# Kernel tuning notes

Measured on AMD Instinct MI355X. Metric: run time of the kernel, lower is better.

The kernel has to match this reference:

```python
import jax, jax.numpy as jnp
import numpy as np

CUBE_LEN = 512
EQU_H = 1024
EQU_W = 2 * EQU_H
EQU_COUNT = 4
CHANNELS = 3


def _rodrigues(r):
    th = np.linalg.norm(r)
    if th < 1e-12:
        return np.eye(3)
    k = r / th
    K = np.array([[0.0, -k[2], k[1]], [k[2], 0.0, -k[0]], [-k[1], k[0], 0.0]])
    return np.eye(3) + np.sin(th) * K + (1.0 - np.cos(th)) * (K @ K)


def _build_lut(L, equ_h):
    # Identical math to Cube2Equirec.__init__/_intersection, fused into
    # per-pixel face id + per-pixel cube-face pixel coordinates (u, v).
    equ_w = equ_h * 2
    theta = (np.arange(equ_w) / (equ_w - 1) - 0.5) * 2 * np.pi
    phi = (np.arange(equ_h) / (equ_h - 1) - 0.5) * np.pi
    theta, phi = np.meshgrid(theta, phi)
    x = np.sin(theta) * np.cos(phi)
    y = np.sin(phi)
    z = np.cos(theta) * np.cos(phi)
    xyz = np.stack([x, y, z], axis=-1)  # [H, W, 3]
    planes = np.array([[0, 0, 1, -1], [1, 0, 0, -1], [0, 0, 1, 1],
                       [1, 0, 0, 1], [0, 1, 0, 1], [0, 1, 0, -1]], dtype=np.float64)
    r_lst = np.array([[0, 0, 0], [0, -0.5, 0], [0, 1, 0],
                      [0, 0.5, 0], [-0.5, 0, 0], [0.5, 0, 0]]) * np.pi
    f = L / 2.0
    K = np.array([[f, 0, (L - 1) / 2.0], [0, f, (L - 1) / 2.0], [0, 0, 1]])
    R_lst = np.stack([_rodrigues(r) for r in r_lst])  # [6, 3, 3]

    abc = planes[:, :3]
    with np.errstate(divide='ignore'):
        depth = -planes[:, 3][None, None, :] / (xyz @ abc.T)  # [H, W, 6]
    depth[depth < 0] = np.inf
    arg = np.argmin(depth, axis=-1)            # per-pixel face id
    dmin = np.min(depth, axis=-1)
    pts = dmin[..., None] * xyz                # intersection points
    Rs = R_lst[arg]                            # [H, W, 3, 3]
    proj = np.einsum('ij,hwjk,hwk->hwi', K, Rs, pts)  # K @ R @ pts
    uv = np.clip(proj[..., :2] / proj[..., 2:3], 0, L - 1)
    return uv.astype(np.float32), arg.astype(np.int32)


def setup_inputs() -> dict:
    key = jax.random.key(0)
    x = jax.random.normal(key, (6 * EQU_COUNT, CHANNELS, CUBE_LEN, CUBE_LEN),
                          dtype=jnp.float32)
    uv_np, face_np = _build_lut(CUBE_LEN, EQU_H)
    return {"x": x, "uv": jnp.asarray(uv_np), "face_idx": jnp.asarray(face_np)}


def _cube2equirec(x, uv, face_idx):
    # x: [6*E, C, L, L]; grid_sample(mode='bilinear', align_corners=True)
    # with grid = (uv/(L-1) - 0.5)*2 samples exactly at pixel coords uv.
    E6, C, L, _ = x.shape
    E = E6 // 6
    xr = x.reshape(E, 6, C, L, L)
    H, W = face_idx.shape
    f = face_idx.reshape(-1)                 # [N]
    u = uv[..., 0].reshape(-1)               # [N], in [0, L-1]
    v = uv[..., 1].reshape(-1)

    x0 = jnp.clip(jnp.floor(u).astype(jnp.int32), 0, L - 1)
    y0 = jnp.clip(jnp.floor(v).astype(jnp.int32), 0, L - 1)
    x1 = jnp.minimum(x0 + 1, L - 1)
    y1 = jnp.minimum(y0 + 1, L - 1)
    wx = (u - x0.astype(u.dtype))[:, None, None]  # [N,1,1]
    wy = (v - y0.astype(v.dtype))[:, None, None]

    def g(yy, xx):
        # advanced indices at axes 1,3,4 -> result [N, E, C]
        return xr[:, f, :, yy, xx]

    out = (g(y0, x0) * (1 - wx) * (1 - wy)
           + g(y0, x1) * wx * (1 - wy)
           + g(y1, x0) * (1 - wx) * wy
           + g(y1, x1) * wx * wy)              # [N, E, C]
    return jnp.transpose(out, (1, 2, 0)).reshape(E, C, H, W)


def reference(x, uv, face_idx):
    return _cube2equirec(x, uv, face_idx)
```

## Files before the change

kernel.cpp:

```cpp
#include <hip/hip_runtime.h>
#include <stdint.h>

#define EQU_H 1024
#define EQU_W 2048
#define HW (EQU_H * EQU_W)

typedef float f32x4 __attribute__((ext_vector_type(4)));
typedef float f32x2 __attribute__((ext_vector_type(2)));

#define IMG_OFF(i)  ((uint64_t)(((i) / 3) * 18874368u + ((i) % 3) * 1048576u))
#define IMG_FOFF(i) (((i) / 3) * 4718592 + ((i) % 3) * 262144)

__device__ __forceinline__ int wave_min(int v) {
#pragma unroll
    for (int o = 32; o; o >>= 1) v = min(v, __shfl_xor(v, o));
    return v;
}
__device__ __forceinline__ int wave_max(int v) {
#pragma unroll
    for (int o = 32; o; o >>= 1) v = max(v, __shfl_xor(v, o));
    return v;
}

__global__ __launch_bounds__(256, 1) void cube2equirec_kernel(
    const float* __restrict__ x,
    const float* __restrict__ uv,
    const int*   __restrict__ face,
    float*       __restrict__ out)
{
    __shared__ float slds[3][2048];
    __shared__ int   sred[24];

    const int tx = blockIdx.x & 63;
    const int ty = blockIdx.x >> 6;
    const int pr = threadIdx.x & 15;
    const int rw = threadIdx.x >> 4;
    const int w  = tx * 32 + pr * 2;
    const int h  = ty * 16 + rw;
    const int idx  = h * EQU_W + w;
    const int pidx = idx >> 1;

    const f32x4 uv4 = ((const f32x4*)uv)[pidx];
    const int2  fpr = ((const int2*)face)[pidx];
    const float uA = uv4.x, vA = uv4.y, uB = uv4.z, vB = uv4.w;
    const int   fA = fpr.x, fB = fpr.y;

    int x0A = (int)floorf(uA), y0A = (int)floorf(vA);
    int x0B = (int)floorf(uB), y0B = (int)floorf(vB);
    x0A = min(max(x0A, 0), 510); y0A = min(max(y0A, 0), 510);
    x0B = min(max(x0B, 0), 510); y0B = min(max(y0B, 0), 510);
    const float wxA = uA - (float)x0A, wyA = vA - (float)y0A;
    const float wxB = uB - (float)x0B, wyB = vB - (float)y0B;

    int fmn = min(fA, fB),   fmx = max(fA, fB);
    int xmn = min(x0A, x0B), xmx = max(x0A, x0B);
    int ymn = min(y0A, y0B), ymx = max(y0A, y0B);
    fmn = wave_min(fmn); fmx = wave_max(fmx);
    xmn = wave_min(xmn); xmx = wave_max(xmx);
    ymn = wave_min(ymn); ymx = wave_max(ymx);
    const int wid = threadIdx.x >> 6, lane = threadIdx.x & 63;
    if (lane == 0) {
        int* p = &sred[wid * 6];
        p[0] = fmn; p[1] = fmx; p[2] = xmn; p[3] = xmx; p[4] = ymn; p[5] = ymx;
    }
    __syncthreads();
#pragma unroll
    for (int ww = 0; ww < 4; ++ww) {
        const int* p = &sred[ww * 6];
        fmn = min(fmn, p[0]); fmx = max(fmx, p[1]);
        xmn = min(xmn, p[2]); xmx = max(xmx, p[3]);
        ymn = min(ymn, p[4]); ymx = max(ymx, p[5]);
    }

    const int  xs     = min(xmn & ~3, 448);
    const bool staged = (fmn == fmx) && ((xmx + 1 - xs) <= 63)
                                     && ((ymx - ymn) <= 29);
    const uint64_t xb = (uint64_t)x;

    if (staged) {
        const int R  = ymx + 2 - ymn;
        const int nu = R << 4;
        const float w00A = (1.f - wxA) * (1.f - wyA), w01A = wxA * (1.f - wyA);
        const float w10A = (1.f - wxA) * wyA,         w11A = wxA * wyA;
        const float w00B = (1.f - wxB) * (1.f - wyB), w01B = wxB * (1.f - wyB);
        const float w10B = (1.f - wxB) * wyB,         w11B = wxB * wyB;
        const int lA = ((y0A - ymn) << 6) + (x0A - xs);
        const int lB = ((y0B - ymn) << 6) + (x0B - xs);
        const int fbase = fmn * 786432;

#pragma unroll
        for (int k = 0; k < 4; ++k) {
#pragma unroll
            for (int r = 0; r < 3; ++r) {
                const float* src = x + IMG_FOFF(k * 3 + r) + fbase;
                int u = threadIdx.x;
                if (u < nu) {
                    const int row = u >> 4, c4 = (u & 15) << 2;
                    *((f32x4*)&slds[r][(row << 6) + c4]) =
                        *(const f32x4*)(src + (ymn + row) * 512 + xs + c4);
                }
                u += 256;
                if (u < nu) {
                    const int row = u >> 4, c4 = (u & 15) << 2;
                    *((f32x4*)&slds[r][(row << 6) + c4]) =
                        *(const f32x4*)(src + (ymn + row) * 512 + xs + c4);
                }
            }
            __syncthreads();
#pragma unroll
            for (int r = 0; r < 3; ++r) {
                const int i = k * 3 + r;
                const float* L = slds[r];
                const float a00 = L[lA], a01 = L[lA + 1];
                const float a10 = L[lA + 64], a11 = L[lA + 65];
                const float b00 = L[lB], b01 = L[lB + 1];
                const float b10 = L[lB + 64], b11 = L[lB + 65];
                f32x2 st;
                st.x = a00 * w00A + a01 * w01A + a10 * w10A + a11 * w11A;
                st.y = b00 * w00B + b01 * w01B + b10 * w10B + b11 * w11B;
                __builtin_nontemporal_store(st, (f32x2*)(out + (size_t)i * HW) + pidx);
            }
            __syncthreads();
        }
        return;
    }

    const int  xmw    = min(x0A, x0B);
    const bool compat = (fA == fB) && (y0A == y0B)
                     && ((max(x0A, x0B) - xmw) <= 2);
    const int xm  = min(compat ? xmw : x0A, 508);
    const int oAw = x0A - xm;
    const int oBw = min(max(x0B - xm, 0), 2);

    const uint32_t vbW = (uint32_t)(fA * 3145728 + y0A * 2048 + xm * 4);
    const uint32_t vbB = (uint32_t)(fB * 3145728 + y0B * 2048 + x0B * 4);

    const float aL = 1.f - wxA, aR = wxA;
    const float bL = 1.f - wxB, bR = wxB;
    f32x4 WA, WB;
    WA.x = (oAw == 0) ? aL : 0.f;
    WA.y = (oAw == 0) ? aR : ((oAw == 1) ? aL : 0.f);
    WA.z = (oAw == 2) ? aL : ((oAw == 1) ? aR : 0.f);
    WA.w = (oAw == 2) ? aR : 0.f;
    WB.x = (oBw == 0) ? bL : 0.f;
    WB.y = (oBw == 0) ? bR : ((oBw == 1) ? bL : 0.f);
    WB.z = (oBw == 2) ? bL : ((oBw == 1) ? bR : 0.f);
    WB.w = (oBw == 2) ? bR : 0.f;
    const f32x4 WA0 = WA * (1.f - wyA), WA1 = WA * wyA;
    const f32x4 WB0 = WB * (1.f - wyB), WB1 = WB * wyB;
    const float c00 = bL * (1.f - wyB), c01 = bR * (1.f - wyB);
    const float c10 = bL * wyB,         c11 = bR * wyB;

#define EMIT2(i, R0, R1, Q0, Q1)                                             \
    {                                                                        \
        const float ovA = R0.x * WA0.x + R0.y * WA0.y + R0.z * WA0.z         \
                        + R0.w * WA0.w + R1.x * WA1.x + R1.y * WA1.y         \
                        + R1.z * WA1.z + R1.w * WA1.w;                       \
        const float oBw2 = R0.x * WB0.x + R0.y * WB0.y + R0.z * WB0.z        \
                        + R0.w * WB0.w + R1.x * WB1.x + R1.y * WB1.y         \
                        + R1.z * WB1.z + R1.w * WB1.w;                       \
        const float oBf = Q0.x * c00 + Q0.y * c01 + Q1.x * c10 + Q1.y * c11; \
        f32x2 st;                                                            \
        st.x = ovA;                                                          \
        st.y = compat ? oBw2 : oBf;                                          \
        __builtin_nontemporal_store(st, (f32x2*)(out + (size_t)(i) * HW) + pidx); \
    }

#define ROUND(I0)                                                            \
    {                                                                        \
        f32x4 r0_0, r1_0, r0_1, r1_1, r0_2, r1_2,                            \
              r0_3, r1_3, r0_4, r1_4, r0_5, r1_5;                            \
        asm volatile(                                                        \
            "global_load_dwordx4 %[a0], %[vb], %[s0]\n\t"                    \
            "global_load_dwordx4 %[b0], %[vb], %[s0] offset:2048\n\t"        \
            "global_load_dwordx4 %[a1], %[vb], %[s1]\n\t"                    \
            "global_load_dwordx4 %[b1], %[vb], %[s1] offset:2048\n\t"        \
            "global_load_dwordx4 %[a2], %[vb], %[s2]\n\t"                    \
            "global_load_dwordx4 %[b2], %[vb], %[s2] offset:2048\n\t"        \
            "global_load_dwordx4 %[a3], %[vb], %[s3]\n\t"                    \
            "global_load_dwordx4 %[b3], %[vb], %[s3] offset:2048\n\t"        \
            "global_load_dwordx4 %[a4], %[vb], %[s4]\n\t"                    \
            "global_load_dwordx4 %[b4], %[vb], %[s4] offset:2048\n\t"        \
            "global_load_dwordx4 %[a5], %[vb], %[s5]\n\t"                    \
            "global_load_dwordx4 %[b5], %[vb], %[s5] offset:2048"            \
            : [a0] "=&v"(r0_0), [b0] "=&v"(r1_0),                            \
              [a1] "=&v"(r0_1), [b1] "=&v"(r1_1),                            \
              [a2] "=&v"(r0_2), [b2] "=&v"(r1_2),                            \
              [a3] "=&v"(r0_3), [b3] "=&v"(r1_3),                            \
              [a4] "=&v"(r0_4), [b4] "=&v"(r1_4),                            \
              [a5] "=&v"(r0_5), [b5] "=&v"(r1_5)                             \
            : [vb] "v"(vbW),                                                 \
              [s0] "s"(xb + IMG_OFF((I0) + 0)),                              \
              [s1] "s"(xb + IMG_OFF((I0) + 1)),                              \
              [s2] "s"(xb + IMG_OFF((I0) + 2)),                              \
              [s3] "s"(xb + IMG_OFF((I0) + 3)),                              \
              [s4] "s"(xb + IMG_OFF((I0) + 4)),                              \
              [s5] "s"(xb + IMG_OFF((I0) + 5)));                             \
        f32x2 q0_0 = {0.f, 0.f}, q1_0 = {0.f, 0.f};                          \
        f32x2 q0_1 = {0.f, 0.f}, q1_1 = {0.f, 0.f};                          \
        f32x2 q0_2 = {0.f, 0.f}, q1_2 = {0.f, 0.f};                          \
        f32x2 q0_3 = {0.f, 0.f}, q1_3 = {0.f, 0.f};                          \
        f32x2 q0_4 = {0.f, 0.f}, q1_4 = {0.f, 0.f};                          \
        f32x2 q0_5 = {0.f, 0.f}, q1_5 = {0.f, 0.f};                          \
        if (!compat) {                                                       \
            asm volatile(                                                    \
                "global_load_dwordx2 %[a0], %[vb], %[s0]\n\t"                \
                "global_load_dwordx2 %[b0], %[vb], %[s0] offset:2048\n\t"    \
                "global_load_dwordx2 %[a1], %[vb], %[s1]\n\t"                \
                "global_load_dwordx2 %[b1], %[vb], %[s1] offset:2048\n\t"    \
                "global_load_dwordx2 %[a2], %[vb], %[s2]\n\t"                \
                "global_load_dwordx2 %[b2], %[vb], %[s2] offset:2048\n\t"    \
                "global_load_dwordx2 %[a3], %[vb], %[s3]\n\t"                \
                "global_load_dwordx2 %[b3], %[vb], %[s3] offset:2048\n\t"    \
                "global_load_dwordx2 %[a4], %[vb], %[s4]\n\t"                \
                "global_load_dwordx2 %[b4], %[vb], %[s4] offset:2048\n\t"    \
                "global_load_dwordx2 %[a5], %[vb], %[s5]\n\t"                \
                "global_load_dwordx2 %[b5], %[vb], %[s5] offset:2048"        \
                : [a0] "=&v"(q0_0), [b0] "=&v"(q1_0),                        \
                  [a1] "=&v"(q0_1), [b1] "=&v"(q1_1),                        \
                  [a2] "=&v"(q0_2), [b2] "=&v"(q1_2),                        \
                  [a3] "=&v"(q0_3), [b3] "=&v"(q1_3),                        \
                  [a4] "=&v"(q0_4), [b4] "=&v"(q1_4),                        \
                  [a5] "=&v"(q0_5), [b5] "=&v"(q1_5)                         \
                : [vb] "v"(vbB),                                             \
                  [s0] "s"(xb + IMG_OFF((I0) + 0)),                          \
                  [s1] "s"(xb + IMG_OFF((I0) + 1)),                          \
                  [s2] "s"(xb + IMG_OFF((I0) + 2)),                          \
                  [s3] "s"(xb + IMG_OFF((I0) + 3)),                          \
                  [s4] "s"(xb + IMG_OFF((I0) + 4)),                          \
                  [s5] "s"(xb + IMG_OFF((I0) + 5)));                         \
        }                                                                    \
        asm volatile("s_waitcnt vmcnt(0)" ::: "memory");                     \
        __builtin_amdgcn_sched_barrier(0);                                   \
        EMIT2((I0) + 0, r0_0, r1_0, q0_0, q1_0)                              \
        EMIT2((I0) + 1, r0_1, r1_1, q0_1, q1_1)                              \
        EMIT2((I0) + 2, r0_2, r1_2, q0_2, q1_2)                              \
        EMIT2((I0) + 3, r0_3, r1_3, q0_3, q1_3)                              \
        EMIT2((I0) + 4, r0_4, r1_4, q0_4, q1_4)                              \
        EMIT2((I0) + 5, r0_5, r1_5, q0_5, q1_5)                              \
    }

    ROUND(0)
    ROUND(6)

#undef ROUND
#undef EMIT2
}

extern "C" void kernel_launch(void* const* d_in, const int* in_sizes, int n_in,
                              void* d_out, int out_size, void* d_ws, size_t ws_size,
                              hipStream_t stream) {
    const float* x    = (const float*)d_in[0];
    const float* uv   = (const float*)d_in[1];
    const int*   face = (const int*)d_in[2];
    float*       out  = (float*)d_out;

    const int grid = 64 * 64;
    hipLaunchKernelGGL(cube2equirec_kernel, dim3(grid), dim3(256), 0, stream,
                       x, uv, face, out);
}
```

Before: 217.2 us.

## Stage variable-shape LDS footprints and traverse tiles column-major

The LDS staging path now sizes its footprint to the actual x-extent of the tile (C columns rounded to 4) instead of a fixed 64-wide window. Any footprint up to 400 float4 units can be staged, so more tiles take the LDS path rather than the fallback direct-gather path. Each thread's global and LDS staging offsets are precomputed once outside the channel loop. The block-to-tile mapping is also swapped so consecutive blocks walk down columns, which changes cache locality across neighbouring blocks. The costs are integer divides per thread and possible LDS bank conflicts from non-power-of-two row strides.

New measurement: 214.3 us. Within noise of the previous version (-1.4%).

```diff
diff --git a/kernel.cpp b/kernel.cpp
--- a/kernel.cpp
+++ b/kernel.cpp
@@ -28,17 +28,16 @@
     const int*   __restrict__ face,
     float*       __restrict__ out)
 {
-    __shared__ float slds[3][2048];
+    __shared__ float slds[3][1600];
     __shared__ int   sred[24];
 
-    const int tx = blockIdx.x & 63;
-    const int ty = blockIdx.x >> 6;
+    const int ty = blockIdx.x & 63;
+    const int tx = blockIdx.x >> 6;
     const int pr = threadIdx.x & 15;
     const int rw = threadIdx.x >> 4;
     const int w  = tx * 32 + pr * 2;
     const int h  = ty * 16 + rw;
-    const int idx  = h * EQU_W + w;
-    const int pidx = idx >> 1;
+    const int pidx = (h * EQU_W + w) >> 1;
 
     const f32x4 uv4 = ((const f32x4*)uv)[pidx];
     const int2  fpr = ((const int2*)face)[pidx];
@@ -72,39 +71,40 @@
         ymn = min(ymn, p[4]); ymx = max(ymx, p[5]);
     }
 
-    const int  xs     = min(xmn & ~3, 448);
-    const bool staged = (fmn == fmx) && ((xmx + 1 - xs) <= 63)
-                                     && ((ymx - ymn) <= 29);
+    const int xs = xmn & ~3;
+    const int R  = ymx + 2 - ymn;
+    int C = ((xmx + 2 - xs) + 3) & ~3;
+    C = min(C, 512 - xs);
+    const int  U      = C >> 2;
+    const bool staged = (fmn == fmx) && (U * R <= 400);
     const uint64_t xb = (uint64_t)x;
 
     if (staged) {
-        const int R  = ymx + 2 - ymn;
-        const int nu = R << 4;
+        const int UR = U * R;
+        const int fbase = fmn * 786432;
+        const int u0 = threadIdx.x, u1 = threadIdx.x + 256;
+        const int r0 = u0 / U, c0 = u0 - r0 * U;
+        const int r1 = u1 / U, c1 = u1 - r1 * U;
+        const bool g0 = u0 < UR, g1 = u1 < UR;
+        const int go0 = (ymn + r0) * 512 + xs + (c0 << 2);
+        const int go1 = (ymn + r1) * 512 + xs + (c1 << 2);
+        const int lo0 = r0 * C + (c0 << 2);
+        const int lo1 = r1 * C + (c1 << 2);
+        const int lA = (y0A - ymn) * C + (x0A - xs);
+        const int lB = (y0B - ymn) * C + (x0B - xs);
+
         const float w00A = (1.f - wxA) * (1.f - wyA), w01A = wxA * (1.f - wyA);
         const float w10A = (1.f - wxA) * wyA,         w11A = wxA * wyA;
         const float w00B = (1.f - wxB) * (1.f - wyB), w01B = wxB * (1.f - wyB);
         const float w10B = (1.f - wxB) * wyB,         w11B = wxB * wyB;
-        const int lA = ((y0A - ymn) << 6) + (x0A - xs);
-        const int lB = ((y0B - ymn) << 6) + (x0B - xs);
-        const int fbase = fmn * 786432;
 
 #pragma unroll
         for (int k = 0; k < 4; ++k) {
 #pragma unroll
             for (int r = 0; r < 3; ++r) {
                 const float* src = x + IMG_FOFF(k * 3 + r) + fbase;
-                int u = threadIdx.x;
-                if (u < nu) {
-                    const int row = u >> 4, c4 = (u & 15) << 2;
-                    *((f32x4*)&slds[r][(row << 6) + c4]) =
-                        *(const f32x4*)(src + (ymn + row) * 512 + xs + c4);
-                }
-                u += 256;
-                if (u < nu) {
-                    const int row = u >> 4, c4 = (u & 15) << 2;
-                    *((f32x4*)&slds[r][(row << 6) + c4]) =
-                        *(const f32x4*)(src + (ymn + row) * 512 + xs + c4);
-                }
+                if (g0) *((f32x4*)&slds[r][lo0]) = *(const f32x4*)(src + go0);
+                if (g1) *((f32x4*)&slds[r][lo1]) = *(const f32x4*)(src + go1);
             }
             __syncthreads();
 #pragma unroll
@@ -112,9 +112,9 @@
                 const int i = k * 3 + r;
                 const float* L = slds[r];
                 const float a00 = L[lA], a01 = L[lA + 1];
-                const float a10 = L[lA + 64], a11 = L[lA + 65];
+                const float a10 = L[lA + C], a11 = L[lA + C + 1];
                 const float b00 = L[lB], b01 = L[lB + 1];
-                const float b10 = L[lB + 64], b11 = L[lB + 65];
+                const float b10 = L[lB + C], b11 = L[lB + C + 1];
                 f32x2 st;
                 st.x = a00 * w00A + a01 * w01A + a10 * w10A + a11 * w11A;
                 st.y = b00 * w00B + b01 * w01B + b10 * w10B + b11 * w11B;
```
